# Kernel optimization log

Measured on AMD Instinct MI355X. Metric: run time of the kernel, lower is better.

## Reference

```python
import jax, jax.numpy as jnp
import numpy as np

N = 512          # number of proposals
C = 1024         # in_channels
FLAT = C * 7 * 7 # 50176, fc1 input dim
D = 1024         # hidden / feat_dim / attention dim
SCALE = 1.0 / np.sqrt(float(D))


def setup_inputs() -> dict:
    key = jax.random.key(0)
    ks = jax.random.split(key, 20)
    w = lambda k, shape: (jax.random.normal(k, shape, jnp.float32) * 0.01)
    inp = {"x": jax.random.normal(ks[0], (N, C, 7, 7), jnp.float32)}
    # SelsaHead fc layers
    inp["fc1_w"] = w(ks[1], (D, FLAT)); inp["fc1_b"] = jnp.zeros((D,), jnp.float32)
    inp["fc2_w"] = w(ks[2], (D, D));    inp["fc2_b"] = jnp.zeros((D,), jnp.float32)
    # attention_1 (semantic_aggregation): fc1, fc2, 1x1 conv (stored as [D,D] matrix)
    inp["a1_fc1_w"] = w(ks[3], (D, D)); inp["a1_fc1_b"] = jnp.zeros((D,), jnp.float32)
    inp["a1_fc2_w"] = w(ks[4], (D, D)); inp["a1_fc2_b"] = jnp.zeros((D,), jnp.float32)
    inp["a1_conv_w"] = w(ks[5], (D, D)); inp["a1_conv_b"] = jnp.zeros((D,), jnp.float32)
    # attention_2
    inp["a2_fc1_w"] = w(ks[6], (D, D)); inp["a2_fc1_b"] = jnp.zeros((D,), jnp.float32)
    inp["a2_fc2_w"] = w(ks[7], (D, D)); inp["a2_fc2_b"] = jnp.zeros((D,), jnp.float32)
    inp["a2_conv_w"] = w(ks[8], (D, D)); inp["a2_conv_b"] = jnp.zeros((D,), jnp.float32)
    return inp


def _semantic_aggregation(x, w1, b1, w2, b2, cw, cb):
    # x: [N, D]. Single-head dense attention over proposals, values = x itself.
    q = x @ w1.T + b1                      # [N, D]
    k = x @ w2.T + b2                      # [N, D]
    p = jax.nn.softmax((q @ k.T) * SCALE, axis=-1)  # [N, N]
    out = p @ x                            # [N, D]  (values are raw x)
    return out @ cw.T + cb                 # 1x1 conv == linear [N, D]


def reference(x, fc1_w, fc1_b, fc2_w, fc2_b,
              a1_fc1_w, a1_fc1_b, a1_fc2_w, a1_fc2_b, a1_conv_w, a1_conv_b,
              a2_fc1_w, a2_fc1_b, a2_fc2_w, a2_fc2_b, a2_conv_w, a2_conv_b):
    out = x.reshape(x.shape[0], -1) @ fc1_w.T + fc1_b        # [N, D]
    r1 = _semantic_aggregation(out, a1_fc1_w, a1_fc1_b, a1_fc2_w, a1_fc2_b,
                               a1_conv_w, a1_conv_b)
    h = jax.nn.relu(out + r1)
    h = h @ fc2_w.T + fc2_b                                  # [N, D]
    r2 = _semantic_aggregation(h, a2_fc1_w, a2_fc1_b, a2_fc2_w, a2_fc2_b,
                               a2_conv_w, a2_conv_b)
    return jax.nn.relu(h + r2 + out)                         # [N, D]
```

## Files before the change

kernel.cpp:

```cpp
#include <hip/hip_runtime.h>
#include <hip/hip_bf16.h>

typedef __attribute__((ext_vector_type(8))) short short8;
typedef __attribute__((ext_vector_type(4))) float f32x4;

#define N_PROP 512
#define DHID   1024
#define KFLAT  50176
#define SM_SCALE 0.03125f

__device__ inline short f2bf(float x) {
  __hip_bfloat16 b = __float2bfloat16(x);
  return __builtin_bit_cast(short, b);
}
__device__ inline float bf2f(unsigned short u) {
  unsigned int x = (unsigned int)u << 16;
  return __builtin_bit_cast(float, x);
}

__device__ inline void pinned_bar() {
  asm volatile("s_waitcnt lgkmcnt(0)" ::: "memory");
  __builtin_amdgcn_s_barrier();
  asm volatile("" ::: "memory");
}

__global__ __launch_bounds__(1024, 4)
void gemm_fc1(const float* __restrict__ A, const float* __restrict__ B,
              __hip_bfloat16* __restrict__ parts)
{
  constexpr int BK = 32;
  constexpr int KLEN = 1568, NT = KLEN / BK;
  __shared__ short sA[2][256 * 32];
  __shared__ short sB[2][256 * 32];

  const int n = gridDim.x;
  int lid = blockIdx.x;
  lid = (lid & 7) * (n >> 3) + (lid >> 3);
  const int y    = lid >> 3;
  const int tile = lid & 7;
  const int tm = tile >> 2;
  const int tn = tile & 3;

  const int k0 = y * KLEN;

  const int tid  = threadIdx.x;
  const int lane = tid & 63;
  const int wid  = tid >> 6;
  const int wr = wid >> 2, wc = wid & 3;
  const int l16 = lane & 15, kq = lane >> 4;

  const float* Ab = A + (size_t)(tm * 256) * KFLAT;
  const float* Bb = B + (size_t)(tn * 256) * KFLAT;

  const int srow = tid >> 2;
  const int sc   = tid & 3;
  const int sphys = sc ^ ((srow >> 1) & 3);

  f32x4 acc[4][4];
  #pragma unroll
  for (int i = 0; i < 4; ++i)
    #pragma unroll
    for (int j = 0; j < 4; ++j)
      acc[i][j] = (f32x4){0.f, 0.f, 0.f, 0.f};

  float4 ra0, ra1, rb0, rb1;

  auto loadAB = [&](int kk) {
    const float* pa = Ab + (size_t)srow * KFLAT + kk + sc * 8;
    const float* pb = Bb + (size_t)srow * KFLAT + kk + sc * 8;
    ra0 = *(const float4*)pa; ra1 = *(const float4*)(pa + 4);
    rb0 = *(const float4*)pb; rb1 = *(const float4*)(pb + 4);
  };
  auto storeAB = [&](int b) {
    short8 s;
    s[0]=f2bf(ra0.x); s[1]=f2bf(ra0.y); s[2]=f2bf(ra0.z); s[3]=f2bf(ra0.w);
    s[4]=f2bf(ra1.x); s[5]=f2bf(ra1.y); s[6]=f2bf(ra1.z); s[7]=f2bf(ra1.w);
    *(short8*)&sA[b][srow * 32 + sphys * 8] = s;
    s[0]=f2bf(rb0.x); s[1]=f2bf(rb0.y); s[2]=f2bf(rb0.z); s[3]=f2bf(rb0.w);
    s[4]=f2bf(rb1.x); s[5]=f2bf(rb1.y); s[6]=f2bf(rb1.z); s[7]=f2bf(rb1.w);
    *(short8*)&sB[b][srow * 32 + sphys * 8] = s;
  };
  auto compute = [&](int b) {
    short8 af[4], bf[4];
    #pragma unroll
    for (int i = 0; i < 4; ++i) {
      int R  = wr * 64 + i * 16 + l16;
      int ph = kq ^ ((R >> 1) & 3);
      af[i] = *(short8*)&sA[b][R * 32 + ph * 8];
    }
    #pragma unroll
    for (int j = 0; j < 4; ++j) {
      int R  = wc * 64 + j * 16 + l16;
      int ph = kq ^ ((R >> 1) & 3);
      bf[j] = *(short8*)&sB[b][R * 32 + ph * 8];
    }
    #pragma unroll
    for (int i = 0; i < 4; ++i)
      #pragma unroll
      for (int j = 0; j < 4; ++j)
        acc[i][j] = __builtin_amdgcn_mfma_f32_16x16x32_bf16(af[i], bf[j], acc[i][j], 0, 0, 0);
  };

  loadAB(k0);
  storeAB(0);
  loadAB(k0 + BK);
  pinned_bar();

  int cur = 0;
  for (int t = 0; t < NT; ++t) {
    if (t + 1 < NT) {
      storeAB(cur ^ 1);
      if (t + 2 < NT) loadAB(k0 + (t + 2) * BK);
    }
    compute(cur);
    pinned_bar();
    cur ^= 1;
  }

  __hip_bfloat16* P = parts + (size_t)y * (N_PROP * DHID);
  const int crow0 = tm * 256 + wr * 64;
  const int ccol0 = tn * 256 + wc * 64;
  #pragma unroll
  for (int i = 0; i < 4; ++i)
    #pragma unroll
    for (int j = 0; j < 4; ++j)
      #pragma unroll
      for (int e = 0; e < 4; ++e) {
        int r = crow0 + i * 16 + kq * 4 + e;
        int c = ccol0 + j * 16 + l16;
        P[(size_t)r * DHID + c] = __float2bfloat16(acc[i][j][e]);
      }
}

template<int BM, int BN, int BK, typename BT>
__global__ __launch_bounds__(256, 2)
void gemm_bf(const __hip_bfloat16* __restrict__ A, int lda,
             const BT* __restrict__ B1, const BT* __restrict__ B2, int ldb,
             float* __restrict__ C, __hip_bfloat16* __restrict__ Cb, int ldc,
             int tiles_n, int ktot, size_t c_z_stride,
             const float* __restrict__ bias1, const float* __restrict__ bias2,
             const float* __restrict__ res1, const float* __restrict__ res2,
             __hip_bfloat16* __restrict__ Ct, int ldct, int do_relu)
{
  constexpr int BKP = BK + 8;
  constexpr int WM = BM / 2, WN = BN / 2;
  constexpr int FM = WM / 16, FN = WN / 16;
  constexpr int NC = BK / 8;
  constexpr int NA = (BM * BK) / (8 * 256);
  constexpr int NB = (BN * BK) / (8 * 256);
  constexpr bool BF = sizeof(BT) == 2;

  __shared__ short As[2][BM * BKP];
  __shared__ short Bs[2][BN * BKP];

  const int n = gridDim.x;
  int lid = blockIdx.x;
  lid = (lid & 7) * (n >> 3) + (lid >> 3);
  const int tm = lid / tiles_n;
  const int tn = lid % tiles_n;
  const int nt = ktot / BK;

  if (C)  C  += (size_t)blockIdx.z * c_z_stride;
  if (Cb) Cb += (size_t)blockIdx.z * c_z_stride;
  const BT* B       = blockIdx.z ? B2 : B1;
  const float* bias = blockIdx.z ? bias2 : bias1;

  const int tid  = threadIdx.x;
  const int lane = tid & 63;
  const int wid  = tid >> 6;
  const int wm = wid >> 1, wn = wid & 1;
  const int l16 = lane & 15, kq = lane >> 4;

  const __hip_bfloat16* Ab = A + (size_t)(tm * BM) * lda;
  const BT*             Bb = B + (size_t)(tn * BN) * ldb;

  f32x4 acc[FM][FN];
  #pragma unroll
  for (int i = 0; i < FM; ++i)
    #pragma unroll
    for (int j = 0; j < FN; ++j)
      acc[i][j] = (f32x4){0.f, 0.f, 0.f, 0.f};

  short8 a0[NA]; short8 b0h[NB]; float4 b0f[NB][2];
  short8 a1[NA]; short8 b1h[NB]; float4 b1f[NB][2];

  auto load0 = [&](int kk) {
    #pragma unroll
    for (int i = 0; i < NA; ++i) {
      int ch = tid + i * 256; int r = ch / NC, c = (ch % NC) * 8;
      a0[i] = *(const short8*)(Ab + (size_t)r * lda + kk + c);
    }
    #pragma unroll
    for (int i = 0; i < NB; ++i) {
      int ch = tid + i * 256; int r = ch / NC, c = (ch % NC) * 8;
      if constexpr (BF) b0h[i] = *(const short8*)(Bb + (size_t)r * ldb + kk + c);
      else {
        const float* p = (const float*)Bb + (size_t)r * ldb + kk + c;
        b0f[i][0] = *(const float4*)p; b0f[i][1] = *(const float4*)(p + 4);
      }
    }
  };
  auto load1 = [&](int kk) {
    #pragma unroll
    for (int i = 0; i < NA; ++i) {
      int ch = tid + i * 256; int r = ch / NC, c = (ch % NC) * 8;
      a1[i] = *(const short8*)(Ab + (size_t)r * lda + kk + c);
    }
    #pragma unroll
    for (int i = 0; i < NB; ++i) {
      int ch = tid + i * 256; int r = ch / NC, c = (ch % NC) * 8;
      if constexpr (BF) b1h[i] = *(const short8*)(Bb + (size_t)r * ldb + kk + c);
      else {
        const float* p = (const float*)Bb + (size_t)r * ldb + kk + c;
        b1f[i][0] = *(const float4*)p; b1f[i][1] = *(const float4*)(p + 4);
      }
    }
  };
  auto store0 = [&](int buf) {
    #pragma unroll
    for (int i = 0; i < NA; ++i) {
      int ch = tid + i * 256; int r = ch / NC, c = (ch % NC) * 8;
      *(short8*)&As[buf][r * BKP + c] = a0[i];
    }
    #pragma unroll
    for (int i = 0; i < NB; ++i) {
      int ch = tid + i * 256; int r = ch / NC, c = (ch % NC) * 8;
      if constexpr (BF) *(short8*)&Bs[buf][r * BKP + c] = b0h[i];
      else {
        float4 u = b0f[i][0], v = b0f[i][1];
        short8 w;
        w[0]=f2bf(u.x); w[1]=f2bf(u.y); w[2]=f2bf(u.z); w[3]=f2bf(u.w);
        w[4]=f2bf(v.x); w[5]=f2bf(v.y); w[6]=f2bf(v.z); w[7]=f2bf(v.w);
        *(short8*)&Bs[buf][r * BKP + c] = w;
      }
    }
  };
  auto store1 = [&](int buf) {
    #pragma unroll
    for (int i = 0; i < NA; ++i) {
      int ch = tid + i * 256; int r = ch / NC, c = (ch % NC) * 8;
      *(short8*)&As[buf][r * BKP + c] = a1[i];
    }
    #pragma unroll
    for (int i = 0; i < NB; ++i) {
      int ch = tid + i * 256; int r = ch / NC, c = (ch % NC) * 8;
      if constexpr (BF) *(short8*)&Bs[buf][r * BKP + c] = b1h[i];
      else {
        float4 u = b1f[i][0], v = b1f[i][1];
        short8 w;
        w[0]=f2bf(u.x); w[1]=f2bf(u.y); w[2]=f2bf(u.z); w[3]=f2bf(u.w);
        w[4]=f2bf(v.x); w[5]=f2bf(v.y); w[6]=f2bf(v.z); w[7]=f2bf(v.w);
        *(short8*)&Bs[buf][r * BKP + c] = w;
      }
    }
  };
  auto compute = [&](int buf) {
    #pragma unroll
    for (int ks = 0; ks < BK / 32; ++ks) {
      short8 af[FM], bf[FN];
      #pragma unroll
      for (int i = 0; i < FM; ++i)
        af[i] = *(short8*)&As[buf][(wm * WM + i * 16 + l16) * BKP + ks * 32 + kq * 8];
      #pragma unroll
      for (int j = 0; j < FN; ++j)
        bf[j] = *(short8*)&Bs[buf][(wn * WN + j * 16 + l16) * BKP + ks * 32 + kq * 8];
      #pragma unroll
      for (int i = 0; i < FM; ++i)
        #pragma unroll
        for (int j = 0; j < FN; ++j)
          acc[i][j] = __builtin_amdgcn_mfma_f32_16x16x32_bf16(af[i], bf[j], acc[i][j], 0, 0, 0);
    }
  };

  load0(0);
  store0(0);
  load1(BK);
  pinned_bar();

  int t = 0;
  for (; t + 2 < nt; t += 2) {
    store1(1); load0((t + 2) * BK);
    compute(0); pinned_bar();
    store0(0); load1((t + 3) * BK);
    compute(1); pinned_bar();
  }
  store1(1);
  compute(0); pinned_bar();
  compute(1);

  const int crow0 = tm * BM + wm * WM;
  const int ccol0 = tn * BN + wn * WN;
  #pragma unroll
  for (int i = 0; i < FM; ++i)
    #pragma unroll
    for (int j = 0; j < FN; ++j)
      #pragma unroll
      for (int e = 0; e < 4; ++e) {
        int r = crow0 + i * 16 + kq * 4 + e;
        int c = ccol0 + j * 16 + l16;
        float v = acc[i][j][e];
        if (bias) v += bias[c];
        if (res1) v += res1[(size_t)r * ldc + c];
        if (res2) v += res2[(size_t)r * ldc + c];
        if (do_relu) v = fmaxf(v, 0.f);
        if (C)  C [(size_t)r * ldc + c] = v;
        if (Cb) Cb[(size_t)r * ldc + c] = __float2bfloat16(v);
        if (Ct) Ct[(size_t)c * ldct + r] = __float2bfloat16(v);
      }
}

__global__ __launch_bounds__(256)
void reduce_t(const __hip_bfloat16* __restrict__ parts, const float* __restrict__ bias,
              float* __restrict__ out0f, __hip_bfloat16* __restrict__ out0b,
              __hip_bfloat16* __restrict__ T)
{
  __shared__ float tile[32][33];
  int bx = blockIdx.x * 32;
  int by = blockIdx.y * 32;
  int tc = (threadIdx.x & 7) * 4;
  int tr = threadIdx.x >> 3;
  {
    int r = by + tr, c0 = bx + tc;
    float4 bv = *(const float4*)(bias + c0);
    float s0 = bv.x, s1 = bv.y, s2 = bv.z, s3 = bv.w;
    for (int sl = 0; sl < 32; ++sl) {
      ushort4 u = *(const ushort4*)(parts + (size_t)sl * (N_PROP * DHID) +
                                    (size_t)r * DHID + c0);
      s0 += bf2f(u.x); s1 += bf2f(u.y); s2 += bf2f(u.z); s3 += bf2f(u.w);
    }
    float4 o = {s0, s1, s2, s3};
    *(float4*)(out0f + (size_t)r * DHID + c0) = o;
    ushort4 ob = {(unsigned short)f2bf(s0), (unsigned short)f2bf(s1),
                  (unsigned short)f2bf(s2), (unsigned short)f2bf(s3)};
    *(ushort4*)(out0b + (size_t)r * DHID + c0) = ob;
    tile[tr][tc] = s0; tile[tr][tc + 1] = s1;
    tile[tr][tc + 2] = s2; tile[tr][tc + 3] = s3;
  }
  __syncthreads();
  int tx = threadIdx.x & 31, ty = threadIdx.x >> 5;
  #pragma unroll
  for (int i = 0; i < 4; ++i)
    T[(size_t)(bx + ty + i * 8) * N_PROP + by + tx] =
        __float2bfloat16(tile[tx][ty + i * 8]);
}

__global__ __launch_bounds__(256)
void softmax_rows(const float* __restrict__ x, __hip_bfloat16* __restrict__ p, float scale)
{
  int row = blockIdx.x;
  const float* q = x + (size_t)row * N_PROP;
  int tid = threadIdx.x;
  float a = q[tid] * scale;
  float b = q[tid + 256] * scale;
  float m = fmaxf(a, b);
  #pragma unroll
  for (int o = 32; o > 0; o >>= 1) m = fmaxf(m, __shfl_xor(m, o));
  __shared__ float sm[4], ss[4];
  int w = tid >> 6;
  if ((tid & 63) == 0) sm[w] = m;
  __syncthreads();
  m = fmaxf(fmaxf(sm[0], sm[1]), fmaxf(sm[2], sm[3]));
  float ea = __expf(a - m), eb = __expf(b - m);
  float s = ea + eb;
  #pragma unroll
  for (int o = 32; o > 0; o >>= 1) s += __shfl_xor(s, o);
  if ((tid & 63) == 0) ss[w] = s;
  __syncthreads();
  s = ss[0] + ss[1] + ss[2] + ss[3];
  float inv = 1.f / s;
  p[(size_t)row * N_PROP + tid]       = __float2bfloat16(ea * inv);
  p[(size_t)row * N_PROP + tid + 256] = __float2bfloat16(eb * inv);
}

extern "C" void kernel_launch(void* const* d_in, const int* in_sizes, int n_in,
                              void* d_out, int out_size, void* d_ws, size_t ws_size,
                              hipStream_t stream)
{
  (void)in_sizes; (void)n_in; (void)out_size; (void)ws_size;
  const float* x      = (const float*)d_in[0];
  const float* fc1_w  = (const float*)d_in[1];
  const float* fc1_b  = (const float*)d_in[2];
  const float* fc2_w  = (const float*)d_in[3];
  const float* fc2_b  = (const float*)d_in[4];
  const float* a1w1   = (const float*)d_in[5];
  const float* a1b1   = (const float*)d_in[6];
  const float* a1w2   = (const float*)d_in[7];
  const float* a1b2   = (const float*)d_in[8];
  const float* a1cw   = (const float*)d_in[9];
  const float* a1cb   = (const float*)d_in[10];
  const float* a2w1   = (const float*)d_in[11];
  const float* a2b1   = (const float*)d_in[12];
  const float* a2w2   = (const float*)d_in[13];
  const float* a2b2   = (const float*)d_in[14];
  const float* a2cw   = (const float*)d_in[15];
  const float* a2cb   = (const float*)d_in[16];
  float* out = (float*)d_out;

  typedef __hip_bfloat16 bf16;
  char* ws = (char*)d_ws;
  const size_t MB = 1024 * 1024;
  float* out0f  = (float*)(ws + 0 * MB);
  float* h1f    = (float*)(ws + 2 * MB);
  float* logits = (float*)(ws + 4 * MB);
  bf16*  out0b  = (bf16*)(ws + 5 * MB);
  bf16*  T      = (bf16*)(ws + 6 * MB);
  bf16*  q      = (bf16*)(ws + 7 * MB);
  bf16*  k      = (bf16*)(ws + 8 * MB);
  bf16*  att    = (bf16*)(ws + 9 * MB);
  bf16*  h0b    = (bf16*)(ws + 10 * MB);
  bf16*  h1b    = (bf16*)(ws + 11 * MB);
  bf16*  T2     = (bf16*)(ws + 12 * MB);
  bf16*  pb     = (bf16*)(ws + 13 * MB);
  bf16*  parts  = (bf16*)(ws + 14 * MB);
  const size_t ND = (size_t)N_PROP * DHID;
  dim3 blk(256);

  gemm_fc1<<<dim3(256), dim3(1024), 0, stream>>>(x, fc1_w, parts);
  reduce_t<<<dim3(DHID / 32, N_PROP / 32), blk, 0, stream>>>(
      parts, fc1_b, out0f, out0b, T);

  gemm_bf<32, 64, 128, float><<<dim3(256, 1, 2), blk, 0, stream>>>(
      out0b, DHID, a1w1, a1w2, DHID,
      nullptr, q, DHID, 16, DHID, ND,
      a1b1, a1b2, nullptr, nullptr, nullptr, 0, 0);
  gemm_bf<32, 32, 128, bf16><<<dim3(256), blk, 0, stream>>>(
      q, DHID, k, nullptr, DHID,
      logits, nullptr, N_PROP, 16, DHID, 0,
      nullptr, nullptr, nullptr, nullptr, nullptr, 0, 0);
  softmax_rows<<<N_PROP, blk, 0, stream>>>(logits, pb, SM_SCALE);
  gemm_bf<32, 64, 128, bf16><<<dim3(256), blk, 0, stream>>>(
      pb, N_PROP, T, nullptr, N_PROP,
      nullptr, att, DHID, 16, N_PROP, 0,
      nullptr, nullptr, nullptr, nullptr, nullptr, 0, 0);
  gemm_bf<32, 64, 128, float><<<dim3(256), blk, 0, stream>>>(
      att, DHID, a1cw, nullptr, DHID,
      nullptr, h0b, DHID, 16, DHID, 0,
      a1cb, nullptr, out0f, nullptr, nullptr, 0, 1);
  gemm_bf<32, 64, 128, float><<<dim3(256), blk, 0, stream>>>(
      h0b, DHID, fc2_w, nullptr, DHID,
      h1f, h1b, DHID, 16, DHID, 0,
      fc2_b, nullptr, nullptr, nullptr, T2, N_PROP, 0);

  gemm_bf<32, 64, 128, float><<<dim3(256, 1, 2), blk, 0, stream>>>(
      h1b, DHID, a2w1, a2w2, DHID,
      nullptr, q, DHID, 16, DHID, ND,
      a2b1, a2b2, nullptr, nullptr, nullptr, 0, 0);
  gemm_bf<32, 32, 128, bf16><<<dim3(256), blk, 0, stream>>>(
      q, DHID, k, nullptr, DHID,
      logits, nullptr, N_PROP, 16, DHID, 0,
      nullptr, nullptr, nullptr, nullptr, nullptr, 0, 0);
  softmax_rows<<<N_PROP, blk, 0, stream>>>(logits, pb, SM_SCALE);
  gemm_bf<32, 64, 128, bf16><<<dim3(256), blk, 0, stream>>>(
      pb, N_PROP, T2, nullptr, N_PROP,
      nullptr, att, DHID, 16, N_PROP, 0,
      nullptr, nullptr, nullptr, nullptr, nullptr, 0, 0);
  gemm_bf<32, 64, 128, float><<<dim3(256), blk, 0, stream>>>(
      att, DHID, a2cw, nullptr, DHID,
      out, nullptr, DHID, 16, DHID, 0,
      a2cb, nullptr, h1f, out0f, nullptr, 0, 1);
}
```

Measured before the change: 196.1 us.

## Reassociate attention conv before P@V and fuse into batched projection GEMM

Rewrites (P@x)@Wc^T + b as P@(x@Wc^T + b), which holds because softmax rows sum to one. The conv projection becomes a third z-slice of the Q/K projection GEMM, writing a transposed V, and this removes one GEMM launch per attention block. The fc1 reduction becomes a simple streaming sum with no transpose, and fc1 weight loads use nontemporal hints. Rounding changes slightly because the conv is now applied before the attention matmul, in bf16.

```diff
diff --git a/kernel.cpp b/kernel.cpp
--- a/kernel.cpp
+++ b/kernel.cpp
@@ -63,21 +63,23 @@
     for (int j = 0; j < 4; ++j)
       acc[i][j] = (f32x4){0.f, 0.f, 0.f, 0.f};
 
-  float4 ra0, ra1, rb0, rb1;
+  float4 ra0, ra1;
+  f32x4  rb0, rb1;
 
   auto loadAB = [&](int kk) {
     const float* pa = Ab + (size_t)srow * KFLAT + kk + sc * 8;
     const float* pb = Bb + (size_t)srow * KFLAT + kk + sc * 8;
     ra0 = *(const float4*)pa; ra1 = *(const float4*)(pa + 4);
-    rb0 = *(const float4*)pb; rb1 = *(const float4*)(pb + 4);
+    rb0 = __builtin_nontemporal_load((const f32x4*)pb);
+    rb1 = __builtin_nontemporal_load((const f32x4*)pb + 1);
   };
   auto storeAB = [&](int b) {
     short8 s;
     s[0]=f2bf(ra0.x); s[1]=f2bf(ra0.y); s[2]=f2bf(ra0.z); s[3]=f2bf(ra0.w);
     s[4]=f2bf(ra1.x); s[5]=f2bf(ra1.y); s[6]=f2bf(ra1.z); s[7]=f2bf(ra1.w);
     *(short8*)&sA[b][srow * 32 + sphys * 8] = s;
-    s[0]=f2bf(rb0.x); s[1]=f2bf(rb0.y); s[2]=f2bf(rb0.z); s[3]=f2bf(rb0.w);
-    s[4]=f2bf(rb1.x); s[5]=f2bf(rb1.y); s[6]=f2bf(rb1.z); s[7]=f2bf(rb1.w);
+    s[0]=f2bf(rb0[0]); s[1]=f2bf(rb0[1]); s[2]=f2bf(rb0[2]); s[3]=f2bf(rb0[3]);
+    s[4]=f2bf(rb1[0]); s[5]=f2bf(rb1[1]); s[6]=f2bf(rb1[2]); s[7]=f2bf(rb1[3]);
     *(short8*)&sB[b][srow * 32 + sphys * 8] = s;
   };
   auto compute = [&](int b) {
@@ -135,12 +137,14 @@
 template<int BM, int BN, int BK, typename BT>
 __global__ __launch_bounds__(256, 2)
 void gemm_bf(const __hip_bfloat16* __restrict__ A, int lda,
-             const BT* __restrict__ B1, const BT* __restrict__ B2, int ldb,
+             const BT* __restrict__ B1, const BT* __restrict__ B2,
+             const BT* __restrict__ B3, int ldb,
              float* __restrict__ C, __hip_bfloat16* __restrict__ Cb, int ldc,
              int tiles_n, int ktot, size_t c_z_stride,
              const float* __restrict__ bias1, const float* __restrict__ bias2,
+             const float* __restrict__ bias3,
              const float* __restrict__ res1, const float* __restrict__ res2,
-             __hip_bfloat16* __restrict__ Ct, int ldct, int do_relu)
+             __hip_bfloat16* __restrict__ Ct, int ldct, int ct_z, int do_relu)
 {
   constexpr int BKP = BK + 8;
   constexpr int WM = BM / 2, WN = BN / 2;
@@ -162,8 +166,9 @@
 
   if (C)  C  += (size_t)blockIdx.z * c_z_stride;
   if (Cb) Cb += (size_t)blockIdx.z * c_z_stride;
-  const BT* B       = blockIdx.z ? B2 : B1;
-  const float* bias = blockIdx.z ? bias2 : bias1;
+  const BT* B       = blockIdx.z == 0 ? B1 : (blockIdx.z == 1 ? B2 : B3);
+  const float* bias = blockIdx.z == 0 ? bias1 : (blockIdx.z == 1 ? bias2 : bias3);
+  const bool wr_ct  = Ct && ((int)blockIdx.z == ct_z);
 
   const int tid  = threadIdx.x;
   const int lane = tid & 63;
@@ -305,43 +310,28 @@
         if (do_relu) v = fmaxf(v, 0.f);
         if (C)  C [(size_t)r * ldc + c] = v;
         if (Cb) Cb[(size_t)r * ldc + c] = __float2bfloat16(v);
-        if (Ct) Ct[(size_t)c * ldct + r] = __float2bfloat16(v);
+        if (wr_ct) Ct[(size_t)c * ldct + r] = __float2bfloat16(v);
       }
 }
 
 __global__ __launch_bounds__(256)
-void reduce_t(const __hip_bfloat16* __restrict__ parts, const float* __restrict__ bias,
-              float* __restrict__ out0f, __hip_bfloat16* __restrict__ out0b,
-              __hip_bfloat16* __restrict__ T)
+void reduce_s(const __hip_bfloat16* __restrict__ parts, const float* __restrict__ bias,
+              float* __restrict__ out0f, __hip_bfloat16* __restrict__ out0b)
 {
-  __shared__ float tile[32][33];
-  int bx = blockIdx.x * 32;
-  int by = blockIdx.y * 32;
-  int tc = (threadIdx.x & 7) * 4;
-  int tr = threadIdx.x >> 3;
-  {
-    int r = by + tr, c0 = bx + tc;
-    float4 bv = *(const float4*)(bias + c0);
-    float s0 = bv.x, s1 = bv.y, s2 = bv.z, s3 = bv.w;
-    for (int sl = 0; sl < 32; ++sl) {
-      ushort4 u = *(const ushort4*)(parts + (size_t)sl * (N_PROP * DHID) +
-                                    (size_t)r * DHID + c0);
-      s0 += bf2f(u.x); s1 += bf2f(u.y); s2 += bf2f(u.z); s3 += bf2f(u.w);
-    }
-    float4 o = {s0, s1, s2, s3};
-    *(float4*)(out0f + (size_t)r * DHID + c0) = o;
-    ushort4 ob = {(unsigned short)f2bf(s0), (unsigned short)f2bf(s1),
-                  (unsigned short)f2bf(s2), (unsigned short)f2bf(s3)};
-    *(ushort4*)(out0b + (size_t)r * DHID + c0) = ob;
-    tile[tr][tc] = s0; tile[tr][tc + 1] = s1;
-    tile[tr][tc + 2] = s2; tile[tr][tc + 3] = s3;
+  int idx4 = blockIdx.x * 256 + threadIdx.x;
+  int c4 = idx4 & (DHID / 4 - 1);
+  float4 b = *(const float4*)(bias + (size_t)c4 * 4);
+  float s0 = b.x, s1 = b.y, s2 = b.z, s3 = b.w;
+  for (int i = 0; i < 32; ++i) {
+    ushort4 u = *(const ushort4*)(parts + (size_t)i * (N_PROP * DHID) +
+                                  (size_t)idx4 * 4);
+    s0 += bf2f(u.x); s1 += bf2f(u.y); s2 += bf2f(u.z); s3 += bf2f(u.w);
   }
-  __syncthreads();
-  int tx = threadIdx.x & 31, ty = threadIdx.x >> 5;
-  #pragma unroll
-  for (int i = 0; i < 4; ++i)
-    T[(size_t)(bx + ty + i * 8) * N_PROP + by + tx] =
-        __float2bfloat16(tile[tx][ty + i * 8]);
+  float4 o = {s0, s1, s2, s3};
+  *(float4*)(out0f + (size_t)idx4 * 4) = o;
+  ushort4 ob = {(unsigned short)f2bf(s0), (unsigned short)f2bf(s1),
+                (unsigned short)f2bf(s2), (unsigned short)f2bf(s3)};
+  *(ushort4*)(out0b + (size_t)idx4 * 4) = ob;
 }
 
 __global__ __launch_bounds__(256)
@@ -403,59 +393,48 @@
   float* h1f    = (float*)(ws + 2 * MB);
   float* logits = (float*)(ws + 4 * MB);
   bf16*  out0b  = (bf16*)(ws + 5 * MB);
-  bf16*  T      = (bf16*)(ws + 6 * MB);
+  bf16*  h0b    = (bf16*)(ws + 6 * MB);
   bf16*  q      = (bf16*)(ws + 7 * MB);
   bf16*  k      = (bf16*)(ws + 8 * MB);
-  bf16*  att    = (bf16*)(ws + 9 * MB);
-  bf16*  h0b    = (bf16*)(ws + 10 * MB);
+  bf16*  Vt     = (bf16*)(ws + 10 * MB);
   bf16*  h1b    = (bf16*)(ws + 11 * MB);
-  bf16*  T2     = (bf16*)(ws + 12 * MB);
-  bf16*  pb     = (bf16*)(ws + 13 * MB);
-  bf16*  parts  = (bf16*)(ws + 14 * MB);
+  bf16*  pb     = (bf16*)(ws + 12 * MB);
+  bf16*  parts  = (bf16*)(ws + 13 * MB);
   const size_t ND = (size_t)N_PROP * DHID;
   dim3 blk(256);
 
   gemm_fc1<<<dim3(256), dim3(1024), 0, stream>>>(x, fc1_w, parts);
-  reduce_t<<<dim3(DHID / 32, N_PROP / 32), blk, 0, stream>>>(
-      parts, fc1_b, out0f, out0b, T);
-
-  gemm_bf<32, 64, 128, float><<<dim3(256, 1, 2), blk, 0, stream>>>(
-      out0b, DHID, a1w1, a1w2, DHID,
+  reduce_s<<<dim3(512), blk, 0, stream>>>(parts, fc1_b, out0f, out0b);
+
+  gemm_bf<32, 64, 128, float><<<dim3(256, 1, 3), blk, 0, stream>>>(
+      out0b, DHID, a1w1, a1w2, a1cw, DHID,
       nullptr, q, DHID, 16, DHID, ND,
-      a1b1, a1b2, nullptr, nullptr, nullptr, 0, 0);
+      a1b1, a1b2, a1cb, nullptr, nullptr, Vt, N_PROP, 2, 0);
   gemm_bf<32, 32, 128, bf16><<<dim3(256), blk, 0, stream>>>(
-      q, DHID, k, nullptr, DHID,
+      q, DHID, k, nullptr, nullptr, DHID,
       logits, nullptr, N_PROP, 16, DHID, 0,
-      nullptr, nullptr, nullptr, nullptr, nullptr, 0, 0);
+      nullptr, nullptr, nullptr, nullptr, nullptr, nullptr, 0, -1, 0);
   softmax_rows<<<N_PROP, blk, 0, stream>>>(logits, pb, SM_SCALE);
   gemm_bf<32, 64, 128, bf16><<<dim3(256), blk, 0, stream>>>(
-      pb, N_PROP, T, nullptr, N_PROP,
-      nullptr, att, DHID, 16, N_PROP, 0,
-      nullptr, nullptr, nullptr, nullptr, nullptr, 0, 0);
+      pb, N_PROP, Vt, nullptr, nullptr, N_PROP,
+      nullptr, h0b, DHID, 16, N_PROP, 0,
+      nullptr, nullptr, nullptr, out0f, nullptr, nullptr, 0, -1, 1);
   gemm_bf<32, 64, 128, float><<<dim3(256), blk, 0, stream>>>(
-      att, DHID, a1cw, nullptr, DHID,
-      nullptr, h0b, DHID, 16, DHID, 0,
-      a1cb, nullptr, out0f, nullptr, nullptr, 0, 1);
-  gemm_bf<32, 64, 128, float><<<dim3(256), blk, 0, stream>>>(
-      h0b, DHID, fc2_w, nullptr, DHID,
+      h0b, DHID, fc2_w, nullptr, nullptr, DHID,
       h1f, h1b, DHID, 16, DHID, 0,
-      fc2_b, nullptr, nullptr, nullptr, T2, N_PROP, 0);
-
-  gemm_bf<32, 64, 128, float><<<dim3(256, 1, 2), blk, 0, stream>>>(
-      h1b, DHID, a2w1, a2w2, DHID,
+      fc2_b, nullptr, nullptr, nullptr, nullptr, nullptr, 0, -1, 0);
+
+  gemm_bf<32, 64, 128, float><<<dim3(256, 1, 3), blk, 0, stream>>>(
+      h1b, DHID, a2w1, a2w2, a2cw, DHID,
       nullptr, q, DHID, 16, DHID, ND,
-      a2b1, a2b2, nullptr, nullptr, nullptr, 0, 0);
+      a2b1, a2b2, a2cb, nullptr, nullptr, Vt, N_PROP, 2, 0);
   gemm_bf<32, 32, 128, bf16><<<dim3(256), blk, 0, stream>>>(
-      q, DHID, k, nullptr, DHID,
+      q, DHID, k, nullptr, nullptr, DHID,
       logits, nullptr, N_PROP, 16, DHID, 0,
-      nullptr, nullptr, nullptr, nullptr, nullptr, 0, 0);
+      nullptr, nullptr, nullptr, nullptr, nullptr, nullptr, 0, -1, 0);
   softmax_rows<<<N_PROP, blk, 0, stream>>>(logits, pb, SM_SCALE);
   gemm_bf<32, 64, 128, bf16><<<dim3(256), blk, 0, stream>>>(
-      pb, N_PROP, T2, nullptr, N_PROP,
-      nullptr, att, DHID, 16, N_PROP, 0,
-      nullptr, nullptr, nullptr, nullptr, nullptr, 0, 0);
-  gemm_bf<32, 64, 128, float><<<dim3(256), blk, 0, stream>>>(
-      att, DHID, a2cw, nullptr, DHID,
-      out, nullptr, DHID, 16, DHID, 0,
-      a2cb, nullptr, h1f, out0f, nullptr, 0, 1);
-}
+      pb, N_PROP, Vt, nullptr, nullptr, N_PROP,
+      out, nullptr, DHID, 16, N_PROP, 0,
+      nullptr, nullptr, nullptr, h1f, out0f, nullptr, 0, -1, 1);
+}
```

After: 185.5 us. -5.4%, faster.
